# Kernel tuning notes

Measured on AMD Instinct MI355X. Metric: run time of the kernel, lower is better.

## Reference

```python
import jax, jax.numpy as jnp
import numpy as np

IRR_IN = 4
IRR_OUT = 4
N_SCALAR = 64
E = 1_000_000
DIM = IRR_IN * IRR_OUT * 2  # 32
HID = 2 * DIM               # 64

# ir_1: swap-pair gather index [1,0,3,2,5,4,7,6]
IR_1 = np.concatenate([np.array([1, 0]) + 2 * i for i in range(IRR_IN)])
# ir_2: alternating sign [1,-1,1,-1,...]
IR_2 = np.ones(2 * IRR_IN, dtype=np.float32)
IR_2[1::2] = -1.0


def setup_inputs() -> dict:
    key = jax.random.key(0)
    ks = jax.random.split(key, 4)
    x = jax.random.normal(ks[0], (E, IRR_IN, 2), dtype=jnp.float32)
    s = jax.random.normal(ks[1], (E, N_SCALAR), dtype=jnp.float32)
    W1 = jax.random.normal(ks[2], (N_SCALAR, HID), dtype=jnp.float32) * (1.0 / np.sqrt(N_SCALAR))
    b1 = jnp.zeros((HID,), dtype=jnp.float32)
    W2 = jax.random.normal(ks[3], (HID, DIM), dtype=jnp.float32) * (1.0 / np.sqrt(HID))
    b2 = jnp.zeros((DIM,), dtype=jnp.float32)
    return {"x": x, "s": s, "W1": W1, "b1": b1, "W2": W2, "b2": b2}


def reference(x, s, W1, b1, W2, b2):
    ir1 = jnp.asarray(IR_1)
    ir2 = jnp.asarray(IR_2)
    # per-edge MLP producing raw weights: [E, irr_out, 2*irr_in]
    h = jax.nn.relu(s @ W1 + b1)
    w = (h @ W2 + b2).reshape(-1, IRR_OUT, 2 * IRR_IN)
    w_1 = w[:, :, ir1]        # pair-swapped copy
    w_2 = w * ir2             # sign-alternated copy
    # stack -> [E, 2, irr_out, 2*irr_in]; permute -> [E, 2*irr_in, irr_out, 2]
    wm = jnp.stack((w_2, w_1), axis=1).transpose(0, 3, 2, 1)
    wm = wm.reshape(-1, 2 * IRR_IN, 2 * IRR_OUT)  # [E, 2*irr_in, 2*irr_out]
    xf = x.reshape(-1, 2 * IRR_IN)                # [E, 2*irr_in]
    out = jnp.einsum('ei,eio->eo', xf, wm)        # tiny per-edge matvec
    return out.reshape(-1, IRR_OUT, 2)
```

## Files before the change

kernel.cpp:

```cpp
#include <hip/hip_runtime.h>
#include <hip/hip_bf16.h>

typedef __bf16 bf16x8 __attribute__((ext_vector_type(8)));
typedef __bf16 bf16x4 __attribute__((ext_vector_type(4)));
typedef float  f32x4  __attribute__((ext_vector_type(4)));
typedef float  f32x2  __attribute__((ext_vector_type(2)));

#define MFMA16(A, B, C) __builtin_amdgcn_mfma_f32_16x16x32_bf16(A, B, C, 0, 0, 0)
#define FENCE_WAIT() do { asm volatile("s_waitcnt lgkmcnt(0)" ::: "memory"); \
                          __builtin_amdgcn_sched_barrier(0); } while (0)
#define FENCE_COMPILER() asm volatile("" ::: "memory")

__global__ __launch_bounds__(256, 4) void so2_fused_kernel(
    const float* __restrict__ x, const float* __restrict__ s,
    const float* __restrict__ W1, const float* __restrict__ b1v,
    const float* __restrict__ W2, const float* __restrict__ b2v,
    float* __restrict__ out, int E)
{
  __shared__ unsigned short lds_w1t[64 * 64];
  __shared__ unsigned short lds_w2t[32 * 64];
  __shared__ char lds_h[4][2048];

  const int tid  = threadIdx.x;
  const int wid  = tid >> 6;
  const int lane = tid & 63;
  const int lrow = lane & 15;
  const int lg   = lane >> 4;

  f32x4 bias1[4], bias2[2];
  #pragma unroll
  for (int jt = 0; jt < 4; ++jt) bias1[jt] = *(const f32x4*)(b1v + jt * 16 + lg * 4);
  #pragma unroll
  for (int dt = 0; dt < 2; ++dt) bias2[dt] = *(const f32x4*)(b2v + dt * 16 + lg * 4);

  #pragma unroll
  for (int it = 0; it < 4; ++it) {
    int i = (it * 256 + tid) * 4;
    f32x4 v = *(const f32x4*)(W1 + i);
    int k = i >> 6, j = i & 63;
    #pragma unroll
    for (int q = 0; q < 4; ++q) {
      int byte = ((j + q) << 7) + (k << 1);
      byte ^= ((j + q) & 7) << 4;
      *(unsigned short*)((char*)lds_w1t + byte) =
          __builtin_bit_cast(unsigned short, (__bf16)v[q]);
    }
  }
  #pragma unroll
  for (int it = 0; it < 2; ++it) {
    int i = (it * 256 + tid) * 4;
    f32x4 v = *(const f32x4*)(W2 + i);
    int k = i >> 5, d = i & 31;
    #pragma unroll
    for (int q = 0; q < 4; ++q) {
      int byte = ((d + q) << 7) + (k << 1);
      byte ^= ((d + q) & 7) << 4;
      *(unsigned short*)((char*)lds_w2t + byte) =
          __builtin_bit_cast(unsigned short, (__bf16)v[q]);
    }
  }
  __syncthreads();

  bf16x8 w2f[2][2];
  #pragma unroll
  for (int dt = 0; dt < 2; ++dt)
    #pragma unroll
    for (int c = 0; c < 2; ++c) {
      int d = dt * 16 + lrow;
      int byte = (d << 7) + ((c * 32 + lg * 8) << 1);
      byte ^= (d & 7) << 4;
      w2f[dt][c] = *(const bf16x8*)((const char*)lds_w2t + byte);
    }

  const int wbase = blockIdx.x * 1024 + wid * 256;
  const int rem = E - wbase;
  const int nt = rem <= 0 ? 0 : (rem >= 256 ? 16 : ((rem + 15) >> 4));
  if (nt == 0) return;

  char* hbuf = lds_h[wid];

  f32x4 sN[4];
  f32x4 xN;
  {
    int er = wbase + lrow; er = er < E ? er : E - 1;
    const float* sp = s + (size_t)er * 64 + lg * 8;
    sN[0] = *(const f32x4*)(sp);
    sN[1] = *(const f32x4*)(sp + 4);
    sN[2] = *(const f32x4*)(sp + 32);
    sN[3] = *(const f32x4*)(sp + 36);
    xN = *(const f32x4*)(x + (size_t)er * 8 + (lg & 1) * 4);
  }

  for (int t = 0; t < nt; ++t) {
    const int ebase = wbase + t * 16;

    bf16x8 sf0, sf1;
    #pragma unroll
    for (int i = 0; i < 4; ++i) {
      sf0[i] = (__bf16)sN[0][i]; sf0[i + 4] = (__bf16)sN[1][i];
      sf1[i] = (__bf16)sN[2][i]; sf1[i + 4] = (__bf16)sN[3][i];
    }
    const f32x4 xe = xN;

    {
      int er = ebase + 16 + lrow; er = er < E ? er : E - 1;
      const float* sp = s + (size_t)er * 64 + lg * 8;
      sN[0] = *(const f32x4*)(sp);
      sN[1] = *(const f32x4*)(sp + 4);
      sN[2] = *(const f32x4*)(sp + 32);
      sN[3] = *(const f32x4*)(sp + 36);
      xN = *(const f32x4*)(x + (size_t)er * 8 + (lg & 1) * 4);
    }

    #pragma unroll
    for (int jt = 0; jt < 4; ++jt) {
      const int j = jt * 16 + lrow;
      int wb0 = (j << 7) + ((lg * 8) << 1);      wb0 ^= (j & 7) << 4;
      int wb1 = (j << 7) + ((32 + lg * 8) << 1); wb1 ^= (j & 7) << 4;
      bf16x8 wf0 = *(const bf16x8*)((const char*)lds_w1t + wb0);
      bf16x8 wf1 = *(const bf16x8*)((const char*)lds_w1t + wb1);
      f32x4 acc = bias1[jt];
      acc = MFMA16(wf0, sf0, acc);
      acc = MFMA16(wf1, sf1, acc);
      bf16x4 hv;
      #pragma unroll
      for (int r = 0; r < 4; ++r) hv[r] = (__bf16)fmaxf(acc[r], 0.f);
      int byte = (lrow << 7) + ((jt * 16 + lg * 4) << 1);
      byte ^= (lrow & 7) << 4;
      *(bf16x4*)(hbuf + byte) = hv;
    }

    FENCE_WAIT();

    bf16x8 hf0, hf1;
    {
      int b0 = (lrow << 7) + ((lg * 8) << 1);      b0 ^= (lrow & 7) << 4;
      int b1 = (lrow << 7) + ((32 + lg * 8) << 1); b1 ^= (lrow & 7) << 4;
      hf0 = *(const bf16x8*)(hbuf + b0);
      hf1 = *(const bf16x8*)(hbuf + b1);
    }
    FENCE_COMPILER();

    float qr[2], qi[2];
    #pragma unroll
    for (int dt = 0; dt < 2; ++dt) {
      f32x4 a = bias2[dt];
      a = MFMA16(w2f[dt][0], hf0, a);
      a = MFMA16(w2f[dt][1], hf1, a);
      float pr = xe[0] * a[0] - xe[1] * a[1] + xe[2] * a[2] - xe[3] * a[3];
      float pi = xe[0] * a[1] + xe[1] * a[0] + xe[2] * a[3] + xe[3] * a[2];
      qr[dt] = pr + __shfl_xor(pr, 16, 64);
      qi[dt] = pi + __shfl_xor(pi, 16, 64);
    }
    const int sel = lg & 1;
    const int o = (lg >> 1) + 2 * sel;
    const float vr = sel ? qr[1] : qr[0];
    const float vi = sel ? qi[1] : qi[0];
    const int e = ebase + lrow;
    if (e < E) {
      f32x2 v2 = {vr, vi};
      *(f32x2*)(out + (size_t)e * 8 + o * 2) = v2;
    }
  }
}

extern "C" void kernel_launch(void* const* d_in, const int* in_sizes, int n_in,
                              void* d_out, int out_size, void* d_ws, size_t ws_size,
                              hipStream_t stream) {
  const float* x  = (const float*)d_in[0];
  const float* s  = (const float*)d_in[1];
  const float* W1 = (const float*)d_in[2];
  const float* b1 = (const float*)d_in[3];
  const float* W2 = (const float*)d_in[4];
  const float* b2 = (const float*)d_in[5];
  float* out = (float*)d_out;
  const int E = in_sizes[0] / 8;
  const int blocks = (E + 1023) / 1024;
  so2_fused_kernel<<<blocks, 256, 0, stream>>>(x, s, W1, b1, W2, b2, out, E);
}
```

Measured before the change: 64.97 us.

## Use persistent grid of 1024 blocks with interleaved tile assignment and nontemporal memory ops

Replaces one block per 1024 edges with a fixed grid of at most 1024 blocks. Each block takes a contiguous range of 16-edge tiles, and its four waves stride through that range interleaved. All streaming loads of s and x and the output stores become nontemporal. The aim is to amortise the per-block W1/W2 LDS setup over more work, balance tail work, and avoid cache pollution from single-use data. The cost is lower available parallelism per CU (about 4 blocks per CU on 256 CUs) and possibly less latency hiding.

```diff
diff --git a/kernel.cpp b/kernel.cpp
--- a/kernel.cpp
+++ b/kernel.cpp
@@ -72,27 +72,29 @@
       w2f[dt][c] = *(const bf16x8*)((const char*)lds_w2t + byte);
     }
 
-  const int wbase = blockIdx.x * 1024 + wid * 256;
-  const int rem = E - wbase;
-  const int nt = rem <= 0 ? 0 : (rem >= 256 ? 16 : ((rem + 15) >> 4));
-  if (nt == 0) return;
+  const int nTiles = (E + 15) >> 4;
+  const int G = gridDim.x;
+  const int Tb = (int)(((long long)blockIdx.x * nTiles) / G);
+  const int Te = (int)(((long long)(blockIdx.x + 1) * nTiles) / G);
+  const int nLocal = Te - Tb;
+  if (wid >= nLocal) return;
 
   char* hbuf = lds_h[wid];
 
   f32x4 sN[4];
   f32x4 xN;
   {
-    int er = wbase + lrow; er = er < E ? er : E - 1;
+    int er = (Tb + wid) * 16 + lrow; er = er < E ? er : E - 1;
     const float* sp = s + (size_t)er * 64 + lg * 8;
-    sN[0] = *(const f32x4*)(sp);
-    sN[1] = *(const f32x4*)(sp + 4);
-    sN[2] = *(const f32x4*)(sp + 32);
-    sN[3] = *(const f32x4*)(sp + 36);
-    xN = *(const f32x4*)(x + (size_t)er * 8 + (lg & 1) * 4);
+    sN[0] = __builtin_nontemporal_load((const f32x4*)(sp));
+    sN[1] = __builtin_nontemporal_load((const f32x4*)(sp + 4));
+    sN[2] = __builtin_nontemporal_load((const f32x4*)(sp + 32));
+    sN[3] = __builtin_nontemporal_load((const f32x4*)(sp + 36));
+    xN = __builtin_nontemporal_load((const f32x4*)(x + (size_t)er * 8 + (lg & 1) * 4));
   }
 
-  for (int t = 0; t < nt; ++t) {
-    const int ebase = wbase + t * 16;
+  for (int l = wid; l < nLocal; l += 4) {
+    const int ebase = (Tb + l) * 16;
 
     bf16x8 sf0, sf1;
     #pragma unroll
@@ -103,13 +105,14 @@
     const f32x4 xe = xN;
 
     {
-      int er = ebase + 16 + lrow; er = er < E ? er : E - 1;
+      const int nl = (l + 4 < nLocal) ? l + 4 : l;
+      int er = (Tb + nl) * 16 + lrow; er = er < E ? er : E - 1;
       const float* sp = s + (size_t)er * 64 + lg * 8;
-      sN[0] = *(const f32x4*)(sp);
-      sN[1] = *(const f32x4*)(sp + 4);
-      sN[2] = *(const f32x4*)(sp + 32);
-      sN[3] = *(const f32x4*)(sp + 36);
-      xN = *(const f32x4*)(x + (size_t)er * 8 + (lg & 1) * 4);
+      sN[0] = __builtin_nontemporal_load((const f32x4*)(sp));
+      sN[1] = __builtin_nontemporal_load((const f32x4*)(sp + 4));
+      sN[2] = __builtin_nontemporal_load((const f32x4*)(sp + 32));
+      sN[3] = __builtin_nontemporal_load((const f32x4*)(sp + 36));
+      xN = __builtin_nontemporal_load((const f32x4*)(x + (size_t)er * 8 + (lg & 1) * 4));
     }
 
     #pragma unroll
@@ -159,7 +162,7 @@
     const int e = ebase + lrow;
     if (e < E) {
       f32x2 v2 = {vr, vi};
-      *(f32x2*)(out + (size_t)e * 8 + o * 2) = v2;
+      __builtin_nontemporal_store(v2, (f32x2*)(out + (size_t)e * 8 + o * 2));
     }
   }
 }
@@ -175,6 +178,7 @@
   const float* b2 = (const float*)d_in[5];
   float* out = (float*)d_out;
   const int E = in_sizes[0] / 8;
-  const int blocks = (E + 1023) / 1024;
+  const int nTiles = (E + 15) / 16;
+  const int blocks = nTiles < 1024 ? nTiles : 1024;
   so2_fused_kernel<<<blocks, 256, 0, stream>>>(x, s, W1, b1, W2, b2, out, E);
 }
```

Result: slower. 78.23 us (+20.4%).

## Use persistent grid with balanced tile ranges and double-buffered prefetch

Applied to the files above, without the earlier changes.

Replaces the fixed 1024-edges-per-block grid with a grid capped at 1024 blocks, in which each wave processes a contiguous, evenly balanced range of 16-edge tiles. The single-tile register prefetch becomes two-deep, with loads issued two tiles ahead, to hide more global-memory latency. It also amortizes the per-block cost of converting W1/W2 into LDS over more tiles. The trade-offs are higher register pressure from two buffered tiles and fewer resident waves to hide latency.

```diff
diff --git a/kernel.cpp b/kernel.cpp
--- a/kernel.cpp
+++ b/kernel.cpp
@@ -10,6 +10,21 @@
 #define FENCE_WAIT() do { asm volatile("s_waitcnt lgkmcnt(0)" ::: "memory"); \
                           __builtin_amdgcn_sched_barrier(0); } while (0)
 #define FENCE_COMPILER() asm volatile("" ::: "memory")
+
+struct TileRegs { f32x4 s0, s1, s2, s3; f32x4 x; };
+
+__device__ __forceinline__ void load_tile(TileRegs& T, const float* __restrict__ s,
+                                          const float* __restrict__ x,
+                                          int tile, int lrow, int lg, int E)
+{
+  int er = tile * 16 + lrow; er = er < E ? er : E - 1;
+  const float* sp = s + (size_t)er * 64 + lg * 8;
+  T.s0 = *(const f32x4*)(sp);
+  T.s1 = *(const f32x4*)(sp + 4);
+  T.s2 = *(const f32x4*)(sp + 32);
+  T.s3 = *(const f32x4*)(sp + 36);
+  T.x  = *(const f32x4*)(x + (size_t)er * 8 + (lg & 1) * 4);
+}
 
 __global__ __launch_bounds__(256, 4) void so2_fused_kernel(
     const float* __restrict__ x, const float* __restrict__ s,
@@ -72,45 +87,24 @@
       w2f[dt][c] = *(const bf16x8*)((const char*)lds_w2t + byte);
     }
 
-  const int wbase = blockIdx.x * 1024 + wid * 256;
-  const int rem = E - wbase;
-  const int nt = rem <= 0 ? 0 : (rem >= 256 ? 16 : ((rem + 15) >> 4));
-  if (nt == 0) return;
+  const int nTiles = (E + 15) >> 4;
+  const int W = gridDim.x * 4;
+  const int w = blockIdx.x * 4 + wid;
+  const int Tb = (int)(((long long)w * nTiles) / W);
+  const int Te = (int)(((long long)(w + 1) * nTiles) / W);
+  const int n = Te - Tb;
+  if (n <= 0) return;
 
   char* hbuf = lds_h[wid];
 
-  f32x4 sN[4];
-  f32x4 xN;
-  {
-    int er = wbase + lrow; er = er < E ? er : E - 1;
-    const float* sp = s + (size_t)er * 64 + lg * 8;
-    sN[0] = *(const f32x4*)(sp);
-    sN[1] = *(const f32x4*)(sp + 4);
-    sN[2] = *(const f32x4*)(sp + 32);
-    sN[3] = *(const f32x4*)(sp + 36);
-    xN = *(const f32x4*)(x + (size_t)er * 8 + (lg & 1) * 4);
-  }
-
-  for (int t = 0; t < nt; ++t) {
-    const int ebase = wbase + t * 16;
-
+  auto compute_store = [&](const TileRegs& T, int tile) {
     bf16x8 sf0, sf1;
     #pragma unroll
     for (int i = 0; i < 4; ++i) {
-      sf0[i] = (__bf16)sN[0][i]; sf0[i + 4] = (__bf16)sN[1][i];
-      sf1[i] = (__bf16)sN[2][i]; sf1[i + 4] = (__bf16)sN[3][i];
+      sf0[i] = (__bf16)T.s0[i]; sf0[i + 4] = (__bf16)T.s1[i];
+      sf1[i] = (__bf16)T.s2[i]; sf1[i + 4] = (__bf16)T.s3[i];
     }
-    const f32x4 xe = xN;
-
-    {
-      int er = ebase + 16 + lrow; er = er < E ? er : E - 1;
-      const float* sp = s + (size_t)er * 64 + lg * 8;
-      sN[0] = *(const f32x4*)(sp);
-      sN[1] = *(const f32x4*)(sp + 4);
-      sN[2] = *(const f32x4*)(sp + 32);
-      sN[3] = *(const f32x4*)(sp + 36);
-      xN = *(const f32x4*)(x + (size_t)er * 8 + (lg & 1) * 4);
-    }
+    const f32x4 xe = T.x;
 
     #pragma unroll
     for (int jt = 0; jt < 4; ++jt) {
@@ -156,12 +150,34 @@
     const int o = (lg >> 1) + 2 * sel;
     const float vr = sel ? qr[1] : qr[0];
     const float vi = sel ? qi[1] : qi[0];
-    const int e = ebase + lrow;
+    const int e = tile * 16 + lrow;
     if (e < E) {
       f32x2 v2 = {vr, vi};
       *(f32x2*)(out + (size_t)e * 8 + o * 2) = v2;
     }
+  };
+
+  TileRegs A, B;
+  load_tile(A, s, x, Tb, lrow, lg, E);
+  load_tile(B, s, x, Tb + (n > 1 ? 1 : 0), lrow, lg, E);
+
+  int i = 0;
+  for (; i + 1 < n; i += 2) {
+    TileRegs tA = A;
+    {
+      int nx = i + 2 < n ? i + 2 : n - 1;
+      load_tile(A, s, x, Tb + nx, lrow, lg, E);
+    }
+    compute_store(tA, Tb + i);
+
+    TileRegs tB = B;
+    {
+      int nx = i + 3 < n ? i + 3 : n - 1;
+      load_tile(B, s, x, Tb + nx, lrow, lg, E);
+    }
+    compute_store(tB, Tb + i + 1);
   }
+  if (i < n) compute_store(A, Tb + i);
 }
 
 extern "C" void kernel_launch(void* const* d_in, const int* in_sizes, int n_in,
@@ -175,6 +191,8 @@
   const float* b2 = (const float*)d_in[5];
   float* out = (float*)d_out;
   const int E = in_sizes[0] / 8;
-  const int blocks = (E + 1023) / 1024;
+  const int nTiles = (E + 15) / 16;
+  const int maxBlocks = 1024;
+  const int blocks = (nTiles + 3) / 4 < maxBlocks ? (nTiles + 3) / 4 : maxBlocks;
   so2_fused_kernel<<<blocks, 256, 0, stream>>>(x, s, W1, b1, W2, b2, out, E);
 }
```

New measurement: 107.3 us. 1.65x slower.
